# Kernel optimization log

Hardware: AMD Instinct MI355X
Metric: run time of the kernel (lower is better)

The kernel has to match this reference:

```python
import jax, jax.numpy as jnp
import numpy as np

R = 1
K = 2 * R + 1  # 3x3 kernel -> 8 neighbors


def setup_inputs() -> dict:
    key = jax.random.key(0)
    x = jax.random.normal(key, (8, 128, 224, 224), dtype=jnp.float32)
    return {"x": x}


def reference(x):
    # NFPPooling with measure='norm', p=1, similarity=True, stride=1,
    # padding=0, dilation=1. The frozen ternary grouped conv computes
    # (center - neighbor_k) per channel; LA.norm(ord=1, dim=1) then sums
    # |diff| over channels, yielding [N, 8, H-2, W-2]; negate (similarity).
    B, C, H, W = x.shape
    Ho, Wo = H - (K - 1), W - (K - 1)
    center = x[:, :, R:R + Ho, R:R + Wo]  # [B, C, Ho, Wo]
    # 8 neighbor offsets (row-major cartesian product, center excluded) --
    # same ordering as torch.cartesian_prod with the middle row removed.
    offsets = [(di, dj) for di in range(K) for dj in range(K)
               if not (di == R and dj == R)]
    # Reduce over channels per offset to avoid the [B, C, 8, Ho, Wo]
    # intermediate that the torch grouped conv materializes.
    outs = [jnp.sum(jnp.abs(center - x[:, :, di:di + Ho, dj:dj + Wo]), axis=1)
            for di, dj in offsets]
    out = jnp.stack(outs, axis=1)  # [B, 8, Ho, Wo]
    return -out  # similarity=True
```

## Files before the change

kernel.cpp:

```cpp
#include <hip/hip_runtime.h>
#include <stdint.h>


constexpr int C = 128;
constexpr int H = 224;
constexpr int W = 224;
constexpr int HO = 222;
constexpr int WO = 222;
constexpr int PLANE = H * W;
constexpr int OPLANE = HO * WO;
constexpr int RP = HO / 2;
constexpr int NBLK = 8 * RP;
constexpr int CHW = 32;

struct ChRegs { float4 r0a, r0b, r1a, r1b, r2a, r2b, r3a, r3b; };

__device__ __forceinline__ void loadch(ChRegs& S, const float* p, int nb) {
    S.r0a = *reinterpret_cast<const float4*>(p);
    S.r0b = *reinterpret_cast<const float4*>(p + nb);
    S.r1a = *reinterpret_cast<const float4*>(p + W);
    S.r1b = *reinterpret_cast<const float4*>(p + W + nb);
    S.r2a = *reinterpret_cast<const float4*>(p + 2 * W);
    S.r2b = *reinterpret_cast<const float4*>(p + 2 * W + nb);
    S.r3a = *reinterpret_cast<const float4*>(p + 3 * W);
    S.r3b = *reinterpret_cast<const float4*>(p + 3 * W + nb);
}

__device__ __forceinline__ void compch(const ChRegs& S,
                                       float (&acc0)[8][4], float (&acc1)[8][4]) {
    float v0[8] = {S.r0a.x, S.r0a.y, S.r0a.z, S.r0a.w, S.r0b.x, S.r0b.y, S.r0b.z, S.r0b.w};
    float v1[8] = {S.r1a.x, S.r1a.y, S.r1a.z, S.r1a.w, S.r1b.x, S.r1b.y, S.r1b.z, S.r1b.w};
    float v2[8] = {S.r2a.x, S.r2a.y, S.r2a.z, S.r2a.w, S.r2b.x, S.r2b.y, S.r2b.z, S.r2b.w};
    float v3[8] = {S.r3a.x, S.r3a.y, S.r3a.z, S.r3a.w, S.r3b.x, S.r3b.y, S.r3b.z, S.r3b.w};
    float hh1[5], hh2[5], DR[5], DL[5], Vv[5];
#pragma unroll
    for (int k = 0; k < 5; ++k) {
        hh1[k] = __builtin_fabsf(v1[k + 1] - v1[k]);
        hh2[k] = __builtin_fabsf(v2[k + 1] - v2[k]);
        DR[k]  = __builtin_fabsf(v1[k + 1] - v2[k]);
        DL[k]  = __builtin_fabsf(v1[k] - v2[k + 1]);
        Vv[k]  = __builtin_fabsf(v1[k + 1] - v2[k + 1]);
    }
#pragma unroll
    for (int q = 0; q < 4; ++q) {
        float c1 = v1[q + 1], c2 = v2[q + 1];
        acc0[0][q] += __builtin_fabsf(c1 - v0[q]);
        acc0[1][q] += __builtin_fabsf(c1 - v0[q + 1]);
        acc0[2][q] += __builtin_fabsf(c1 - v0[q + 2]);
        acc0[3][q] += hh1[q];
        acc0[4][q] += hh1[q + 1];
        acc0[5][q] += DR[q];
        acc0[6][q] += Vv[q];
        acc0[7][q] += DL[q + 1];
        acc1[0][q] += DL[q];
        acc1[1][q] += Vv[q];
        acc1[2][q] += DR[q + 1];
        acc1[3][q] += hh2[q];
        acc1[4][q] += hh2[q + 1];
        acc1[5][q] += __builtin_fabsf(c2 - v3[q]);
        acc1[6][q] += __builtin_fabsf(c2 - v3[q + 1]);
        acc1[7][q] += __builtin_fabsf(c2 - v3[q + 2]);
    }
}

__global__ __launch_bounds__(256, 1)
void nfp_sad_kernel(const float* __restrict__ x, float* __restrict__ out) {
    __shared__ float red[3][64][65];

    int b  = blockIdx.x / RP;
    int rp = blockIdx.x % RP;
    int w = threadIdx.x >> 6;
    int l = threadIdx.x & 63;

    float acc0[8][4], acc1[8][4];
#pragma unroll
    for (int o = 0; o < 8; ++o)
#pragma unroll
        for (int q = 0; q < 4; ++q) { acc0[o][q] = 0.0f; acc1[o][q] = 0.0f; }

    if (l < 56) {
        const float* p = x + (size_t)(b * C + w * CHW) * PLANE
                           + (size_t)(2 * rp) * W + 4 * l;
        const int nb = (l == 55) ? 0 : 4;

        ChRegs A, B;
        loadch(A, p, nb); p += PLANE;
        for (int k = 0; k < (CHW - 2) / 2; ++k) {
            loadch(B, p, nb); p += PLANE;
            compch(A, acc0, acc1);
            loadch(A, p, nb); p += PLANE;
            compch(B, acc0, acc1);
        }
        loadch(B, p, nb);
        compch(A, acc0, acc1);
        compch(B, acc0, acc1);

        if (w != 0) {
#pragma unroll
            for (int o = 0; o < 8; ++o)
#pragma unroll
                for (int q = 0; q < 4; ++q) {
                    red[w - 1][l][o * 4 + q]      = acc0[o][q];
                    red[w - 1][l][32 + o * 4 + q] = acc1[o][q];
                }
        }
    }
    __syncthreads();

    if (w == 0 && l < 56) {
#pragma unroll
        for (int o = 0; o < 8; ++o)
#pragma unroll
            for (int q = 0; q < 4; ++q) {
                acc0[o][q] += red[0][l][o * 4 + q] + red[1][l][o * 4 + q]
                            + red[2][l][o * 4 + q];
                acc1[o][q] += red[0][l][32 + o * 4 + q] + red[1][l][32 + o * 4 + q]
                            + red[2][l][32 + o * 4 + q];
            }

        float* ob = out + (size_t)b * 8 * OPLANE + (size_t)(2 * rp) * WO + 4 * l;
#pragma unroll
        for (int o = 0; o < 8; ++o) {
            float* op0 = ob + (size_t)o * OPLANE;
            float* op1 = op0 + WO;
            *reinterpret_cast<float2*>(op0) = make_float2(-acc0[o][0], -acc0[o][1]);
            *reinterpret_cast<float2*>(op1) = make_float2(-acc1[o][0], -acc1[o][1]);
            if (l < 55) {
                *reinterpret_cast<float2*>(op0 + 2) = make_float2(-acc0[o][2], -acc0[o][3]);
                *reinterpret_cast<float2*>(op1 + 2) = make_float2(-acc1[o][2], -acc1[o][3]);
            }
        }
    }
}

extern "C" void kernel_launch(void* const* d_in, const int* in_sizes, int n_in,
                              void* d_out, int out_size, void* d_ws, size_t ws_size,
                              hipStream_t stream) {
    const float* x = (const float*)d_in[0];
    float* out = (float*)d_out;
    nfp_sad_kernel<<<NBLK, 256, 0, stream>>>(x, out);
}
```

Baseline: 65.09 us.

## Stage channel tiles in LDS via async global_load_lds double buffering

Each block now owns four output rows of one image and walks all 128 channels in groups of four. Each group's six input rows are loaded straight into a double-buffered LDS tile with global_load_lds, so the next group's transfer overlaps compute on the current one. Each thread then computes a 2x2 output patch from LDS, which removes the old cross-wave shared-memory reduction. In exchange, input rows are re-read 1.5x instead of 2x, a barrier runs every round, and fewer blocks (448) run with 222 of 256 threads active.

```diff
diff --git a/kernel.cpp b/kernel.cpp
--- a/kernel.cpp
+++ b/kernel.cpp
@@ -9,126 +9,136 @@
 constexpr int WO = 222;
 constexpr int PLANE = H * W;
 constexpr int OPLANE = HO * WO;
-constexpr int RP = HO / 2;
-constexpr int NBLK = 8 * RP;
-constexpr int CHW = 32;
+constexpr int KC = 4;
+constexpr int ROUNDS = C / KC;
+constexpr int TROWS = 4;
+constexpr int SROWS = 6;
+constexpr int NT = 56;
+constexpr int NBLK = 8 * NT;
+constexpr int SLOTS = KC * SROWS * (W / 4);
 
-struct ChRegs { float4 r0a, r0b, r1a, r1b, r2a, r2b, r3a, r3b; };
-
-__device__ __forceinline__ void loadch(ChRegs& S, const float* p, int nb) {
-    S.r0a = *reinterpret_cast<const float4*>(p);
-    S.r0b = *reinterpret_cast<const float4*>(p + nb);
-    S.r1a = *reinterpret_cast<const float4*>(p + W);
-    S.r1b = *reinterpret_cast<const float4*>(p + W + nb);
-    S.r2a = *reinterpret_cast<const float4*>(p + 2 * W);
-    S.r2b = *reinterpret_cast<const float4*>(p + 2 * W + nb);
-    S.r3a = *reinterpret_cast<const float4*>(p + 3 * W);
-    S.r3b = *reinterpret_cast<const float4*>(p + 3 * W + nb);
-}
-
-__device__ __forceinline__ void compch(const ChRegs& S,
-                                       float (&acc0)[8][4], float (&acc1)[8][4]) {
-    float v0[8] = {S.r0a.x, S.r0a.y, S.r0a.z, S.r0a.w, S.r0b.x, S.r0b.y, S.r0b.z, S.r0b.w};
-    float v1[8] = {S.r1a.x, S.r1a.y, S.r1a.z, S.r1a.w, S.r1b.x, S.r1b.y, S.r1b.z, S.r1b.w};
-    float v2[8] = {S.r2a.x, S.r2a.y, S.r2a.z, S.r2a.w, S.r2b.x, S.r2b.y, S.r2b.z, S.r2b.w};
-    float v3[8] = {S.r3a.x, S.r3a.y, S.r3a.z, S.r3a.w, S.r3b.x, S.r3b.y, S.r3b.z, S.r3b.w};
-    float hh1[5], hh2[5], DR[5], DL[5], Vv[5];
-#pragma unroll
-    for (int k = 0; k < 5; ++k) {
-        hh1[k] = __builtin_fabsf(v1[k + 1] - v1[k]);
-        hh2[k] = __builtin_fabsf(v2[k + 1] - v2[k]);
-        DR[k]  = __builtin_fabsf(v1[k + 1] - v2[k]);
-        DL[k]  = __builtin_fabsf(v1[k] - v2[k + 1]);
-        Vv[k]  = __builtin_fabsf(v1[k + 1] - v2[k + 1]);
-    }
-#pragma unroll
-    for (int q = 0; q < 4; ++q) {
-        float c1 = v1[q + 1], c2 = v2[q + 1];
-        acc0[0][q] += __builtin_fabsf(c1 - v0[q]);
-        acc0[1][q] += __builtin_fabsf(c1 - v0[q + 1]);
-        acc0[2][q] += __builtin_fabsf(c1 - v0[q + 2]);
-        acc0[3][q] += hh1[q];
-        acc0[4][q] += hh1[q + 1];
-        acc0[5][q] += DR[q];
-        acc0[6][q] += Vv[q];
-        acc0[7][q] += DL[q + 1];
-        acc1[0][q] += DL[q];
-        acc1[1][q] += Vv[q];
-        acc1[2][q] += DR[q + 1];
-        acc1[3][q] += hh2[q];
-        acc1[4][q] += hh2[q + 1];
-        acc1[5][q] += __builtin_fabsf(c2 - v3[q]);
-        acc1[6][q] += __builtin_fabsf(c2 - v3[q + 1]);
-        acc1[7][q] += __builtin_fabsf(c2 - v3[q + 2]);
-    }
+__device__ __forceinline__ void gload16(const float* g, float* l) {
+    __builtin_amdgcn_global_load_lds(
+        (const __attribute__((address_space(1))) void*)g,
+        (__attribute__((address_space(3))) void*)l, 16, 0, 0);
 }
 
 __global__ __launch_bounds__(256, 1)
 void nfp_sad_kernel(const float* __restrict__ x, float* __restrict__ out) {
-    __shared__ float red[3][64][65];
+    __shared__ float lds[2][SLOTS * 4];
 
-    int b  = blockIdx.x / RP;
-    int rp = blockIdx.x % RP;
-    int w = threadIdx.x >> 6;
-    int l = threadIdx.x & 63;
+    int bid = blockIdx.x;
+    int b = bid & 7;
+    int t = bid >> 3;
+    int i0 = t * TROWS;
+    int tid = threadIdx.x;
 
-    float acc0[8][4], acc1[8][4];
+    const float* xb = x + (size_t)b * C * PLANE;
+    int goff[6];
 #pragma unroll
-    for (int o = 0; o < 8; ++o)
+    for (int j = 0; j < 6; ++j) {
+        int v = j * 256 + tid;
+        int vv = v < SLOTS ? v : SLOTS - 1;
+        int c = vv / 336, rem = vv % 336;
+        int r = rem / 56, k = rem % 56;
+        int row = i0 + r; if (row > H - 1) row = H - 1;
+        goff[j] = c * PLANE + row * W + k * 4;
+    }
+
+    int s = tid;
+    bool act = s < 222;
+    int rp = act ? (s / 111) : 0;
+    int cp = act ? (s % 111) : 0;
+
+    float acc0[8][2], acc1[8][2];
 #pragma unroll
-        for (int q = 0; q < 4; ++q) { acc0[o][q] = 0.0f; acc1[o][q] = 0.0f; }
+    for (int o = 0; o < 8; ++o) {
+        acc0[o][0] = acc0[o][1] = 0.0f;
+        acc1[o][0] = acc1[o][1] = 0.0f;
+    }
 
-    if (l < 56) {
-        const float* p = x + (size_t)(b * C + w * CHW) * PLANE
-                           + (size_t)(2 * rp) * W + 4 * l;
-        const int nb = (l == 55) ? 0 : 4;
+    {
+        float* dst = &lds[0][0];
+#pragma unroll
+        for (int j = 0; j < 5; ++j)
+            gload16(xb + goff[j], dst + (j * 256 + tid) * 4);
+        if (tid < 64) gload16(xb + goff[5], dst + (5 * 256 + tid) * 4);
+    }
 
-        ChRegs A, B;
-        loadch(A, p, nb); p += PLANE;
-        for (int k = 0; k < (CHW - 2) / 2; ++k) {
-            loadch(B, p, nb); p += PLANE;
-            compch(A, acc0, acc1);
-            loadch(A, p, nb); p += PLANE;
-            compch(B, acc0, acc1);
+    int choff = 0;
+    for (int rd = 0; rd < ROUNDS; ++rd) {
+        __syncthreads();
+
+        if (rd + 1 < ROUNDS) {
+            int noff = choff + KC * PLANE;
+            float* dst = &lds[(rd + 1) & 1][0];
+#pragma unroll
+            for (int j = 0; j < 5; ++j)
+                gload16(xb + noff + goff[j], dst + (j * 256 + tid) * 4);
+            if (tid < 64) gload16(xb + noff + goff[5], dst + (5 * 256 + tid) * 4);
         }
-        loadch(B, p, nb);
-        compch(A, acc0, acc1);
-        compch(B, acc0, acc1);
 
-        if (w != 0) {
+        if (act) {
+            const float* Bf = &lds[rd & 1][0];
 #pragma unroll
-            for (int o = 0; o < 8; ++o)
+            for (int c = 0; c < KC; ++c) {
+                const float* pc = Bf + (c * SROWS + 2 * rp) * W + 2 * cp;
+                float v0[4], v1[4], v2[4], v3[4];
+                *(float2*)&v0[0] = *(const float2*)(pc);
+                *(float2*)&v0[2] = *(const float2*)(pc + 2);
+                *(float2*)&v1[0] = *(const float2*)(pc + W);
+                *(float2*)&v1[2] = *(const float2*)(pc + W + 2);
+                *(float2*)&v2[0] = *(const float2*)(pc + 2 * W);
+                *(float2*)&v2[2] = *(const float2*)(pc + 2 * W + 2);
+                *(float2*)&v3[0] = *(const float2*)(pc + 3 * W);
+                *(float2*)&v3[2] = *(const float2*)(pc + 3 * W + 2);
+
+                float hh1[3], hh2[3], DR[3], DL[3], Vv[2];
 #pragma unroll
-                for (int q = 0; q < 4; ++q) {
-                    red[w - 1][l][o * 4 + q]      = acc0[o][q];
-                    red[w - 1][l][32 + o * 4 + q] = acc1[o][q];
+                for (int k = 0; k < 3; ++k) {
+                    hh1[k] = __builtin_fabsf(v1[k + 1] - v1[k]);
+                    hh2[k] = __builtin_fabsf(v2[k + 1] - v2[k]);
+                    DR[k]  = __builtin_fabsf(v1[k + 1] - v2[k]);
+                    DL[k]  = __builtin_fabsf(v1[k] - v2[k + 1]);
                 }
+                Vv[0] = __builtin_fabsf(v1[1] - v2[1]);
+                Vv[1] = __builtin_fabsf(v1[2] - v2[2]);
+
+#pragma unroll
+                for (int q = 0; q < 2; ++q) {
+                    float c1 = v1[q + 1], c2 = v2[q + 1];
+                    acc0[0][q] += __builtin_fabsf(c1 - v0[q]);
+                    acc0[1][q] += __builtin_fabsf(c1 - v0[q + 1]);
+                    acc0[2][q] += __builtin_fabsf(c1 - v0[q + 2]);
+                    acc0[3][q] += hh1[q];
+                    acc0[4][q] += hh1[q + 1];
+                    acc0[5][q] += DR[q];
+                    acc0[6][q] += Vv[q];
+                    acc0[7][q] += DL[q + 1];
+                    acc1[0][q] += DL[q];
+                    acc1[1][q] += Vv[q];
+                    acc1[2][q] += DR[q + 1];
+                    acc1[3][q] += hh2[q];
+                    acc1[4][q] += hh2[q + 1];
+                    acc1[5][q] += __builtin_fabsf(c2 - v3[q]);
+                    acc1[6][q] += __builtin_fabsf(c2 - v3[q + 1]);
+                    acc1[7][q] += __builtin_fabsf(c2 - v3[q + 2]);
+                }
+            }
         }
+        choff += KC * PLANE;
     }
-    __syncthreads();
 
-    if (w == 0 && l < 56) {
-#pragma unroll
-        for (int o = 0; o < 8; ++o)
-#pragma unroll
-            for (int q = 0; q < 4; ++q) {
-                acc0[o][q] += red[0][l][o * 4 + q] + red[1][l][o * 4 + q]
-                            + red[2][l][o * 4 + q];
-                acc1[o][q] += red[0][l][32 + o * 4 + q] + red[1][l][32 + o * 4 + q]
-                            + red[2][l][32 + o * 4 + q];
-            }
-
-        float* ob = out + (size_t)b * 8 * OPLANE + (size_t)(2 * rp) * WO + 4 * l;
+    if (act) {
+        int r0 = i0 + 2 * rp;
+        float* ob = out + (size_t)b * 8 * OPLANE + 2 * cp;
 #pragma unroll
         for (int o = 0; o < 8; ++o) {
-            float* op0 = ob + (size_t)o * OPLANE;
-            float* op1 = op0 + WO;
-            *reinterpret_cast<float2*>(op0) = make_float2(-acc0[o][0], -acc0[o][1]);
-            *reinterpret_cast<float2*>(op1) = make_float2(-acc1[o][0], -acc1[o][1]);
-            if (l < 55) {
-                *reinterpret_cast<float2*>(op0 + 2) = make_float2(-acc0[o][2], -acc0[o][3]);
-                *reinterpret_cast<float2*>(op1 + 2) = make_float2(-acc1[o][2], -acc1[o][3]);
-            }
+            float* op = ob + (size_t)o * OPLANE;
+            if (r0 < HO)
+                *(float2*)(op + (size_t)r0 * WO) = make_float2(-acc0[o][0], -acc0[o][1]);
+            if (r0 + 1 < HO)
+                *(float2*)(op + (size_t)(r0 + 1) * WO) = make_float2(-acc1[o][0], -acc1[o][1]);
         }
     }
 }
```

Measured after the change: 53.03 us. 1.23x faster.
